# Kernel optimization log

Measured on AMD Instinct MI355X. Metric: run time of the kernel, lower is better.

## Reference

```python
import jax, jax.numpy as jnp
import numpy as np

NTOKEN = 64          # vocabulary size
MAX_PREFIX_LEN = 4   # tree depth D
D_MODEL = 648        # >= NTOKEN*(2*D+2) + D + 1 = 645


def setup_inputs() -> dict:
    key = jax.random.key(0)
    S, B = 2048, 8
    src = jax.random.randint(key, (S, B), 0, NTOKEN, dtype=jnp.int32)
    return {"src": src}


def _forward(src):
    n, D, d_model = NTOKEN, MAX_PREFIX_LEN, D_MODEL
    S, B = src.shape
    f32 = jnp.float32
    # shifted[k][t, b] = src[t-k, b] if t >= k else -1.
    # The -1 sentinel reproduces the all-zero one-hot rows the torch code creates
    # by zeroing extended_one_hot[0:i, :, ntoken*i].
    shifted = [src] + [
        jnp.concatenate([jnp.full((k, B), -1, src.dtype), src[: S - k]], axis=0)
        for k in range(1, D + 1)
    ]
    # one-hot blocks for offsets 0..D (sentinel -1 -> all-zero row)
    tok_ids = jnp.arange(n, dtype=src.dtype)
    onehots = [(s[..., None] == tok_ids).astype(f32) for s in shifted]  # each [S,B,n]
    one_hot0 = onehots[0]

    mask = jnp.tril(jnp.ones((S, S), f32), k=-1)  # mask[q, j] = 1 iff j < q

    # Incremental depth-i prefix match: at depth i the torch code compares
    # j_part block m (offset m+1, row j) against i_part block m (offset m, row q)
    # for m = 0..i-1; one-hot vectors are equal iff both tokens equal or both
    # out-of-range, which the sentinel encoding captures exactly.
    match = jnp.ones((S, S, B), bool)
    avg_blocks, count_chans = [], []
    for i in range(1, D + 1):
        match = match & (shifted[i - 1][:, None, :] == shifted[i][None, :, :])
        masked = match.astype(f32) * mask[:, :, None]            # [S(q), S(j), B]
        sums = jnp.einsum('qjb,jbt->qbt', masked, one_hot0)      # matched next-token one-hot sums
        counts = masked.sum(axis=1)[..., None]                   # [S, B, 1]
        avg_blocks.append(sums / jnp.clip(counts, 1))
        count_chans.append(counts)

    # Unconditional causal average over all j < q (exclusive prefix mean)
    cs = jnp.cumsum(one_hot0, axis=0)
    excl = jnp.concatenate([jnp.zeros((1, B, n), f32), cs[:-1]], axis=0)
    q_counts = jnp.broadcast_to(jnp.arange(S, dtype=f32)[:, None, None], (S, B, 1))
    avg_u = excl / jnp.clip(q_counts, 1)

    used = n * (2 * D + 2) + D + 1
    pad = jnp.zeros((S, B, d_model - used), f32)
    # channel layout (matches torch scatter/slice positions exactly):
    #   [0 .. n*(D+1))           one-hot blocks, offsets 0..D
    #   [n*(D+1) .. n*(2D+1))    depth-i matched averages, i=1..D
    #   [n*(2D+1) .. n*(2D+2))   unconditional causal average
    #   n*(2D+2)+i-1             depth-i match counts, i=1..D
    #   n*(2D+2)+D               unconditional count (= q)
    parts = onehots + avg_blocks + [avg_u] + count_chans + [q_counts, pad]
    return jnp.concatenate(parts, axis=-1)


def reference(src):
    return _forward(src)
```

## Files before the change

kernel.cpp:

```cpp
#include <hip/hip_runtime.h>

typedef unsigned long long u64;
typedef unsigned int u32;
typedef unsigned short u16;
typedef unsigned char u8;

#define S_LEN 2048
#define BATCH 8
#define DMODEL 648
#define NBLK 32


__global__ __launch_bounds__(256) void k12_build(const int* __restrict__ src,
                                                 ulonglong2* __restrict__ PAIR,
                                                 u64* __restrict__ PG,
                                                 u16* __restrict__ PB,
                                                 u16* __restrict__ PU,
                                                 u16* __restrict__ PS1,
                                                 u32* __restrict__ RB,
                                                 u8* __restrict__ SRC8) {
    __shared__ __align__(16) ulonglong2 Lpair[2048];
    __shared__ u64 LP[2048];

    const int b = blockIdx.y, gx = blockIdx.x;
    const int tid = threadIdx.x, lane = tid & 63, wv = tid >> 6;

    int myt[8];
    #pragma unroll
    for (int k = 0; k < 8; ++k) {
        const int i = tid + 256 * k;
        myt[k] = src[i * BATCH + b];
        LP[i] = 0;
    }
    __syncthreads();
    #pragma unroll
    for (int k = 0; k < 8; ++k) {
        const int i = tid + 256 * k;
        atomicOr(&LP[(i & ~63) | myt[k]], 1ull << (i & 63));
    }
    __syncthreads();
    #pragma unroll
    for (int k = 0; k < 8; ++k) {
        const int i = tid + 256 * k;
        const u64 m = LP[i];
        const u64 mp = (i >= 64) ? LP[i - 64] : 0ull;
        ulonglong2 pr;
        pr.x = (m << 1) | (mp >> 63);
        pr.y = (m << 2) | (mp >> 62);
        Lpair[i] = pr;
        if (gx == 0) {
            PG[b * 2048 + i] = m;
            PAIR[b * 2048 + i] = pr;
            SRC8[b * 2048 + i] = (u8)myt[k];
        }
    }
    __syncthreads();

    #pragma unroll 1
    for (int j = 0; j < 2; ++j) {
        const int x = gx * 8 + wv * 2 + j;
        u32 cnt = 0, ps1 = 0, rb = 0, pu = 0;
        for (int w = 0; w < NBLK; ++w) {
            const int wb = w << 6;
            const ulonglong2 prx = Lpair[wb + x];
            const u64 pvl = LP[wb + lane];
            const u64 s1l = Lpair[wb + lane].x;
            PB[(size_t)(b * NBLK + w) * 4096 + (x << 6) + lane] = (u16)cnt;
            cnt += (u32)__popcll(prx.x & pvl);
            if (x == 0) { PU[(b * NBLK + w) * 64 + lane] = (u16)pu; pu += (u32)__popcll(pvl); }
            if (lane == 0) PS1[(b * NBLK + w) * 64 + x] = (u16)ps1;
            ps1 += (u32)__popcll(prx.x);
            rb |= ((prx.y & s1l) != 0ull ? 1u : 0u) << w;
        }
        RB[(b << 12) + (x << 6) + lane] = rb;
    }
}

__global__ __launch_bounds__(256) void k3_compute(const ulonglong2* __restrict__ PAIR,
                                                  const u64* __restrict__ PG,
                                                  const u16* __restrict__ PB,
                                                  const u16* __restrict__ PU,
                                                  const u16* __restrict__ PS1,
                                                  const u32* __restrict__ RB,
                                                  const u8* __restrict__ SRC8,
                                                  float* __restrict__ out) {
    const int b = blockIdx.y;
    const int tid = threadIdx.x, lane = tid & 63, wv = tid >> 6;
    const int u = blockIdx.x * 4 + wv;
    const int q0 = u << 1;

    const ulonglong2* PAb = PAIR + b * 2048;
    const u64* PGb  = PG + b * 2048;
    const u16* PBb  = PB + (size_t)b * NBLK * 4096;
    const u16* PUb  = PU + b * 2048;
    const u16* PS1b = PS1 + b * 2048;
    const u32* RBb  = RB + (b << 12);

    const int base = (q0 >= 4) ? (q0 - 4) : 0;
    const u64* sp = (const u64*)(SRC8 + b * 2048 + (base & ~7));
    const u64 lo = sp[0], hi = sp[1];
    const int o = (base & 7) * 8;
    const u64 tb = o ? ((lo >> o) | (hi << (64 - o))) : lo;
    int tk[6];
    #pragma unroll
    for (int i = 0; i < 6; ++i) {
        const int idx = q0 - 4 + i;
        const int bix = idx - base;
        const int sh = (bix > 0 ? bix : 0) * 8;
        tk[i] = (idx >= 0) ? (int)((tb >> sh) & 0xFF) : 0;
    }

    const int cq = q0 >> 6, rem0 = q0 & 63;
    const int cbase = cq << 6;
    const u64 v0 = (1ull << rem0) - 1ull;
    const u64 v1 = (2ull << rem0) - 1ull;

    const u64 pvq = PGb[cbase + lane];
    const int puq = (int)PUb[cbase + lane];
    const ulonglong2 A = PAb[cbase + tk[4]];
    const u64 B1 = PAb[cbase + tk[5]].x;
    const u64 C2 = ((const u64*)&PAb[cbase + tk[3]])[1];
    const int ps1_[2] = {(int)PS1b[cbase + tk[4]], (int)PS1b[cbase + tk[5]]};
    const int hb_[2]  = {(int)PBb[((size_t)cq << 12) + (tk[4] << 6) + lane],
                         (int)PBb[((size_t)cq << 12) + (tk[5] << 6) + lane]};
    const u32 rbm = (1u << cq) - 1u;
    const u32 rare_[2] = {RBb[(tk[3] << 6) + tk[4]] & rbm,
                          RBb[(tk[4] << 6) + tk[5]] & rbm};
    const u64 M1row_[2] = {A.x, B1};
    const u64 S2row_[2] = {C2, A.y};
    const u64 vv_[2] = {v0, v1};

    #pragma unroll
    for (int r = 0; r < 2; ++r) {
        const int q = q0 + r;
        const int t0 = tk[4 + r], t1 = tk[3 + r], t2 = tk[2 + r], t3 = tk[1 + r];
        const u64 valid = vv_[r];

        const u64 M1p = M1row_[r] & valid;
        int c1 = ps1_[r] + __popcll(M1p);
        int h1 = hb_[r] + __popcll(M1p & pvq);
        int cu = puq + __popcll(pvq & valid);

        int c2 = 0, c3 = 0, c4 = 0, h2 = 0, h3 = 0, h4 = 0;
        const u64 M2p = M1p & S2row_[r];
        if (M2p) {
            const u64 cS2  = ((const u64*)&PAb[cbase + t2])[1];
            const u64 cS2p = cq ? ((const u64*)&PAb[cbase - 64 + t2])[1] : 0ull;
            const u64 dS2  = ((const u64*)&PAb[cbase + t3])[1];
            const u64 dS2p = cq ? ((const u64*)&PAb[cbase - 64 + t3])[1] : 0ull;
            const u64 M3p = M2p & ((cS2 << 1) | (cS2p >> 63));
            const u64 M4p = M3p & ((dS2 << 2) | (dS2p >> 62));
            c2 += __popcll(M2p); h2 += __popcll(M2p & pvq);
            c3 += __popcll(M3p); h3 += __popcll(M3p & pvq);
            c4 += __popcll(M4p); h4 += __popcll(M4p & pvq);
        }
        u32 rare = rare_[r];
        while (rare) {
            const int w = __builtin_ctz(rare);
            rare &= rare - 1;
            const int wb = w << 6;
            const u64 M2 = PAb[wb + t0].x & ((const u64*)&PAb[wb + t1])[1];
            const u64 cS2  = ((const u64*)&PAb[wb + t2])[1];
            const u64 cS2p = w ? ((const u64*)&PAb[wb - 64 + t2])[1] : 0ull;
            const u64 dS2  = ((const u64*)&PAb[wb + t3])[1];
            const u64 dS2p = w ? ((const u64*)&PAb[wb - 64 + t3])[1] : 0ull;
            const u64 M3 = M2 & ((cS2 << 1) | (cS2p >> 63));
            const u64 M4 = M3 & ((dS2 << 2) | (dS2p >> 62));
            const u64 pvw = PGb[wb + lane];
            c2 += __popcll(M2); h2 += __popcll(M2 & pvw);
            c3 += __popcll(M3); h3 += __popcll(M3 & pvw);
            c4 += __popcll(M4); h4 += __popcll(M4 & pvw);
        }

        float* op = out + ((size_t)q * BATCH + b) * DMODEL;
        #pragma unroll
        for (int m = 0; m <= 4; ++m) {
            const bool sent = (q - m) < 0;
            op[m * 64 + lane] = (!sent && lane == tk[4 + r - m]) ? 1.f : 0.f;
        }
        op[320 + lane] = (float)h1 / (float)(c1 ? c1 : 1);
        op[384 + lane] = (float)h2 / (float)(c2 ? c2 : 1);
        op[448 + lane] = (float)h3 / (float)(c3 ? c3 : 1);
        op[512 + lane] = (float)h4 / (float)(c4 ? c4 : 1);
        op[576 + lane] = (float)cu / (float)(q ? q : 1);
        if (lane < 8) {
            float v = 0.f;
            if (lane == 0) v = (float)c1;
            else if (lane == 1) v = (float)c2;
            else if (lane == 2) v = (float)c3;
            else if (lane == 3) v = (float)c4;
            else if (lane == 4) v = (float)q;
            op[640 + lane] = v;
        }
    }
}

extern "C" void kernel_launch(void* const* d_in, const int* in_sizes, int n_in,
                              void* d_out, int out_size, void* d_ws, size_t ws_size,
                              hipStream_t stream) {
    const int* src = (const int*)d_in[0];
    float* out = (float*)d_out;
    char* ws = (char*)d_ws;
    ulonglong2* PAIR = (ulonglong2*)(ws);
    u64* PG   = (u64*)(ws + (256u << 10));
    u16* PB   = (u16*)(ws + (384u << 10));
    u16* PU   = (u16*)(ws + (2432u << 10));
    u16* PS1  = (u16*)(ws + (2464u << 10));
    u32* RB   = (u32*)(ws + (2496u << 10));
    u8*  SRC8 = (u8*)(ws + (2624u << 10));

    k12_build<<<dim3(8, BATCH), 256, 0, stream>>>(src, PAIR, PG, PB, PU, PS1, RB, SRC8);
    k3_compute<<<dim3(256, BATCH), 256, 0, stream>>>(PAIR, PG, PB, PU, PS1, RB, SRC8, out);
}
```

Measured before the change: 81.64 us.

## Fuse build and compute kernels into one LDS-resident kernel per 64-row chunk

Merges the table-building kernel and the per-query compute kernel into a single launch. Each block owns one 64-row chunk of one batch and rebuilds the token bitmasks in shared memory. It then computes only that chunk's prefix counts (PB, PS1, PU, RB restricted to earlier chunks), so all lookups hit LDS instead of a global workspace. The goal is to drop the second launch and the global round-trip of the large PB table. The cost is that every one of the 256 blocks redoes the bitmask build, only 256 blocks of 512 threads run, and work is imbalanced across chunks (reversed chunk order partially mitigates this).

After: 83.70 us. +2.5%, slower.

```diff
diff --git a/kernel.cpp b/kernel.cpp
--- a/kernel.cpp
+++ b/kernel.cpp
@@ -8,176 +8,137 @@
 #define S_LEN 2048
 #define BATCH 8
 #define DMODEL 648
-#define NBLK 32
 
-
-__global__ __launch_bounds__(256) void k12_build(const int* __restrict__ src,
-                                                 ulonglong2* __restrict__ PAIR,
-                                                 u64* __restrict__ PG,
-                                                 u16* __restrict__ PB,
-                                                 u16* __restrict__ PU,
-                                                 u16* __restrict__ PS1,
-                                                 u32* __restrict__ RB,
-                                                 u8* __restrict__ SRC8) {
+__global__ __launch_bounds__(512) void fused_kernel(const int* __restrict__ src,
+                                                    float* __restrict__ out) {
     __shared__ __align__(16) ulonglong2 Lpair[2048];
     __shared__ u64 LP[2048];
+    __shared__ u32 RBl[4096];
+    __shared__ u16 PBl[4096];
+    __shared__ u16 PS1l[64];
+    __shared__ u16 PUl[64];
+    __shared__ u8  Ltok[2048];
 
-    const int b = blockIdx.y, gx = blockIdx.x;
-    const int tid = threadIdx.x, lane = tid & 63, wv = tid >> 6;
+    const int b = blockIdx.y;
+    const int c = 31 - blockIdx.x;
+    const int tid = threadIdx.x;
+    const int lane = tid & 63;
+    const int wv = tid >> 6;
 
-    int myt[8];
+    int myt[4];
     #pragma unroll
-    for (int k = 0; k < 8; ++k) {
-        const int i = tid + 256 * k;
+    for (int k = 0; k < 4; ++k) {
+        const int i = tid + 512 * k;
         myt[k] = src[i * BATCH + b];
+        Ltok[i] = (u8)myt[k];
         LP[i] = 0;
     }
     __syncthreads();
     #pragma unroll
-    for (int k = 0; k < 8; ++k) {
-        const int i = tid + 256 * k;
+    for (int k = 0; k < 4; ++k) {
+        const int i = tid + 512 * k;
         atomicOr(&LP[(i & ~63) | myt[k]], 1ull << (i & 63));
     }
     __syncthreads();
     #pragma unroll
-    for (int k = 0; k < 8; ++k) {
-        const int i = tid + 256 * k;
+    for (int k = 0; k < 4; ++k) {
+        const int i = tid + 512 * k;
         const u64 m = LP[i];
         const u64 mp = (i >= 64) ? LP[i - 64] : 0ull;
         ulonglong2 pr;
         pr.x = (m << 1) | (mp >> 63);
         pr.y = (m << 2) | (mp >> 62);
         Lpair[i] = pr;
-        if (gx == 0) {
-            PG[b * 2048 + i] = m;
-            PAIR[b * 2048 + i] = pr;
-            SRC8[b * 2048 + i] = (u8)myt[k];
-        }
     }
     __syncthreads();
 
-    #pragma unroll 1
-    for (int j = 0; j < 2; ++j) {
-        const int x = gx * 8 + wv * 2 + j;
-        u32 cnt = 0, ps1 = 0, rb = 0, pu = 0;
-        for (int w = 0; w < NBLK; ++w) {
+    {
+        u32 pb8[8] = {}, rb8[8] = {};
+        u32 pu = 0;
+        const int tbase = wv << 3;
+        for (int w = 0; w < c; ++w) {
             const int wb = w << 6;
-            const ulonglong2 prx = Lpair[wb + x];
             const u64 pvl = LP[wb + lane];
             const u64 s1l = Lpair[wb + lane].x;
-            PB[(size_t)(b * NBLK + w) * 4096 + (x << 6) + lane] = (u16)cnt;
-            cnt += (u32)__popcll(prx.x & pvl);
-            if (x == 0) { PU[(b * NBLK + w) * 64 + lane] = (u16)pu; pu += (u32)__popcll(pvl); }
-            if (lane == 0) PS1[(b * NBLK + w) * 64 + x] = (u16)ps1;
-            ps1 += (u32)__popcll(prx.x);
-            rb |= ((prx.y & s1l) != 0ull ? 1u : 0u) << w;
+            pu += (u32)__popcll(pvl);
+            #pragma unroll
+            for (int i = 0; i < 8; ++i) {
+                const ulonglong2 pr = Lpair[wb + tbase + i];
+                pb8[i] += (u32)__popcll(pr.x & pvl);
+                rb8[i] |= (u32)((pr.y & s1l) != 0ull) << w;
+            }
         }
-        RB[(b << 12) + (x << 6) + lane] = rb;
+        #pragma unroll
+        for (int i = 0; i < 8; ++i) {
+            PBl[((tbase + i) << 6) + lane] = (u16)pb8[i];
+            RBl[((tbase + i) << 6) + lane] = rb8[i];
+            int s = (int)pb8[i];
+            #pragma unroll
+            for (int sft = 1; sft < 64; sft <<= 1) s += __shfl_xor(s, sft);
+            if (lane == 0) PS1l[tbase + i] = (u16)s;
+        }
+        if (wv == 0) PUl[lane] = (u16)pu;
     }
-}
+    __syncthreads();
 
-__global__ __launch_bounds__(256) void k3_compute(const ulonglong2* __restrict__ PAIR,
-                                                  const u64* __restrict__ PG,
-                                                  const u16* __restrict__ PB,
-                                                  const u16* __restrict__ PU,
-                                                  const u16* __restrict__ PS1,
-                                                  const u32* __restrict__ RB,
-                                                  const u8* __restrict__ SRC8,
-                                                  float* __restrict__ out) {
-    const int b = blockIdx.y;
-    const int tid = threadIdx.x, lane = tid & 63, wv = tid >> 6;
-    const int u = blockIdx.x * 4 + wv;
-    const int q0 = u << 1;
+    const int cbase = c << 6;
+    const u64 pvq = LP[cbase + lane];
+    const int pul = (int)PUl[lane];
 
-    const ulonglong2* PAb = PAIR + b * 2048;
-    const u64* PGb  = PG + b * 2048;
-    const u16* PBb  = PB + (size_t)b * NBLK * 4096;
-    const u16* PUb  = PU + b * 2048;
-    const u16* PS1b = PS1 + b * 2048;
-    const u32* RBb  = RB + (b << 12);
+    #pragma unroll 1
+    for (int k = 0; k < 8; ++k) {
+        const int rem = (wv << 3) + k;
+        const int q = cbase + rem;
+        const u64 valid = (1ull << rem) - 1ull;
 
-    const int base = (q0 >= 4) ? (q0 - 4) : 0;
-    const u64* sp = (const u64*)(SRC8 + b * 2048 + (base & ~7));
-    const u64 lo = sp[0], hi = sp[1];
-    const int o = (base & 7) * 8;
-    const u64 tb = o ? ((lo >> o) | (hi << (64 - o))) : lo;
-    int tk[6];
-    #pragma unroll
-    for (int i = 0; i < 6; ++i) {
-        const int idx = q0 - 4 + i;
-        const int bix = idx - base;
-        const int sh = (bix > 0 ? bix : 0) * 8;
-        tk[i] = (idx >= 0) ? (int)((tb >> sh) & 0xFF) : 0;
-    }
+        const int t4 = (int)Ltok[q];
+        const int t0 = (q >= 1) ? (int)Ltok[q - 1] : 0;
+        const int t1 = (q >= 2) ? (int)Ltok[q - 2] : 0;
+        const int t2 = (q >= 3) ? (int)Ltok[q - 3] : 0;
+        const int t3 = (q >= 4) ? (int)Ltok[q - 4] : 0;
 
-    const int cq = q0 >> 6, rem0 = q0 & 63;
-    const int cbase = cq << 6;
-    const u64 v0 = (1ull << rem0) - 1ull;
-    const u64 v1 = (2ull << rem0) - 1ull;
-
-    const u64 pvq = PGb[cbase + lane];
-    const int puq = (int)PUb[cbase + lane];
-    const ulonglong2 A = PAb[cbase + tk[4]];
-    const u64 B1 = PAb[cbase + tk[5]].x;
-    const u64 C2 = ((const u64*)&PAb[cbase + tk[3]])[1];
-    const int ps1_[2] = {(int)PS1b[cbase + tk[4]], (int)PS1b[cbase + tk[5]]};
-    const int hb_[2]  = {(int)PBb[((size_t)cq << 12) + (tk[4] << 6) + lane],
-                         (int)PBb[((size_t)cq << 12) + (tk[5] << 6) + lane]};
-    const u32 rbm = (1u << cq) - 1u;
-    const u32 rare_[2] = {RBb[(tk[3] << 6) + tk[4]] & rbm,
-                          RBb[(tk[4] << 6) + tk[5]] & rbm};
-    const u64 M1row_[2] = {A.x, B1};
-    const u64 S2row_[2] = {C2, A.y};
-    const u64 vv_[2] = {v0, v1};
-
-    #pragma unroll
-    for (int r = 0; r < 2; ++r) {
-        const int q = q0 + r;
-        const int t0 = tk[4 + r], t1 = tk[3 + r], t2 = tk[2 + r], t3 = tk[1 + r];
-        const u64 valid = vv_[r];
-
-        const u64 M1p = M1row_[r] & valid;
-        int c1 = ps1_[r] + __popcll(M1p);
-        int h1 = hb_[r] + __popcll(M1p & pvq);
-        int cu = puq + __popcll(pvq & valid);
+        const u64 M1p = Lpair[cbase + t0].x & valid;
+        int c1 = (int)PS1l[t0] + __popcll(M1p);
+        int h1 = (int)PBl[(t0 << 6) + lane] + __popcll(M1p & pvq);
+        int cu = pul + __popcll(pvq & valid);
 
         int c2 = 0, c3 = 0, c4 = 0, h2 = 0, h3 = 0, h4 = 0;
-        const u64 M2p = M1p & S2row_[r];
+        const u64 M2p = M1p & Lpair[cbase + t1].y;
         if (M2p) {
-            const u64 cS2  = ((const u64*)&PAb[cbase + t2])[1];
-            const u64 cS2p = cq ? ((const u64*)&PAb[cbase - 64 + t2])[1] : 0ull;
-            const u64 dS2  = ((const u64*)&PAb[cbase + t3])[1];
-            const u64 dS2p = cq ? ((const u64*)&PAb[cbase - 64 + t3])[1] : 0ull;
+            const u64 cS2  = Lpair[cbase + t2].y;
+            const u64 cS2p = c ? Lpair[cbase - 64 + t2].y : 0ull;
+            const u64 dS2  = Lpair[cbase + t3].y;
+            const u64 dS2p = c ? Lpair[cbase - 64 + t3].y : 0ull;
             const u64 M3p = M2p & ((cS2 << 1) | (cS2p >> 63));
             const u64 M4p = M3p & ((dS2 << 2) | (dS2p >> 62));
             c2 += __popcll(M2p); h2 += __popcll(M2p & pvq);
             c3 += __popcll(M3p); h3 += __popcll(M3p & pvq);
             c4 += __popcll(M4p); h4 += __popcll(M4p & pvq);
         }
-        u32 rare = rare_[r];
+        u32 rare = RBl[(t1 << 6) + t0];
         while (rare) {
             const int w = __builtin_ctz(rare);
             rare &= rare - 1;
             const int wb = w << 6;
-            const u64 M2 = PAb[wb + t0].x & ((const u64*)&PAb[wb + t1])[1];
-            const u64 cS2  = ((const u64*)&PAb[wb + t2])[1];
-            const u64 cS2p = w ? ((const u64*)&PAb[wb - 64 + t2])[1] : 0ull;
-            const u64 dS2  = ((const u64*)&PAb[wb + t3])[1];
-            const u64 dS2p = w ? ((const u64*)&PAb[wb - 64 + t3])[1] : 0ull;
+            const u64 M2 = Lpair[wb + t0].x & Lpair[wb + t1].y;
+            const u64 cS2  = Lpair[wb + t2].y;
+            const u64 cS2p = w ? Lpair[wb - 64 + t2].y : 0ull;
+            const u64 dS2  = Lpair[wb + t3].y;
+            const u64 dS2p = w ? Lpair[wb - 64 + t3].y : 0ull;
             const u64 M3 = M2 & ((cS2 << 1) | (cS2p >> 63));
             const u64 M4 = M3 & ((dS2 << 2) | (dS2p >> 62));
-            const u64 pvw = PGb[wb + lane];
+            const u64 pvw = LP[wb + lane];
             c2 += __popcll(M2); h2 += __popcll(M2 & pvw);
             c3 += __popcll(M3); h3 += __popcll(M3 & pvw);
             c4 += __popcll(M4); h4 += __popcll(M4 & pvw);
         }
 
         float* op = out + ((size_t)q * BATCH + b) * DMODEL;
-        #pragma unroll
-        for (int m = 0; m <= 4; ++m) {
-            const bool sent = (q - m) < 0;
-            op[m * 64 + lane] = (!sent && lane == tk[4 + r - m]) ? 1.f : 0.f;
-        }
+        op[0 * 64 + lane] = (lane == t4) ? 1.f : 0.f;
+        op[1 * 64 + lane] = (q >= 1 && lane == t0) ? 1.f : 0.f;
+        op[2 * 64 + lane] = (q >= 2 && lane == t1) ? 1.f : 0.f;
+        op[3 * 64 + lane] = (q >= 3 && lane == t2) ? 1.f : 0.f;
+        op[4 * 64 + lane] = (q >= 4 && lane == t3) ? 1.f : 0.f;
         op[320 + lane] = (float)h1 / (float)(c1 ? c1 : 1);
         op[384 + lane] = (float)h2 / (float)(c2 ? c2 : 1);
         op[448 + lane] = (float)h3 / (float)(c3 ? c3 : 1);
@@ -200,15 +161,5 @@
                               hipStream_t stream) {
     const int* src = (const int*)d_in[0];
     float* out = (float*)d_out;
-    char* ws = (char*)d_ws;
-    ulonglong2* PAIR = (ulonglong2*)(ws);
-    u64* PG   = (u64*)(ws + (256u << 10));
-    u16* PB   = (u16*)(ws + (384u << 10));
-    u16* PU   = (u16*)(ws + (2432u << 10));
-    u16* PS1  = (u16*)(ws + (2464u << 10));
-    u32* RB   = (u32*)(ws + (2496u << 10));
-    u8*  SRC8 = (u8*)(ws + (2624u << 10));
-
-    k12_build<<<dim3(8, BATCH), 256, 0, stream>>>(src, PAIR, PG, PB, PU, PS1, RB, SRC8);
-    k3_compute<<<dim3(256, BATCH), 256, 0, stream>>>(PAIR, PG, PB, PU, PS1, RB, SRC8, out);
+    fused_kernel<<<dim3(32, BATCH), 512, 0, stream>>>(src, out);
 }
```
